# Performance work log

Measured on AMD Instinct MI355X. Metric: run time of the kernel, lower is better.

Reference implementation:

```python
import jax, jax.numpy as jnp
import numpy as np

MARGIN = 0.25
GAMMA = 256.0
NEG_INF = -1e30


def setup_inputs() -> dict:
    key = jax.random.key(0)
    k1, k2 = jax.random.split(key)
    B, D = 8192, 128
    return {
        "embeddings_a": jax.random.normal(k1, (B, D), dtype=jnp.float32),
        "embeddings_b": jax.random.normal(k2, (B, D), dtype=jnp.float32),
    }


def _l2_normalize(x, eps=1e-12):
    # matches F.normalize(p=2, dim=1): x / max(||x||, eps)
    n = jnp.sqrt(jnp.sum(x * x, axis=1, keepdims=True))
    return x / jnp.maximum(n, eps)


def reference(embeddings_a, embeddings_b):
    B = embeddings_a.shape[0]
    a = _l2_normalize(embeddings_a)
    b = _l2_normalize(embeddings_b)
    sim = a @ b.T  # [B, B]

    pos_mask = jnp.eye(B, dtype=bool)  # labels=None path

    # positive logits: -gamma * relu((1-m) - s) * (s - m)
    logit_pos = -GAMMA * jnp.maximum((1.0 - MARGIN) - sim, 0.0) * (sim - MARGIN)
    # negative logits:  gamma * relu(s - m) * (s + m)
    logit_neg = GAMMA * jnp.maximum(sim - MARGIN, 0.0) * (sim + MARGIN)

    # masked per-row logsumexp over positive / negative sets
    lse_pos = jax.nn.logsumexp(jnp.where(pos_mask, logit_pos, NEG_INF), axis=1)
    lse_neg = jax.nn.logsumexp(jnp.where(pos_mask, NEG_INF, logit_neg), axis=1)

    losses = jax.nn.softplus(lse_pos + lse_neg)  # [B]
    return jnp.mean(losses)  # reduction='mean'
```

## Files before the change

### kernel.cpp

```cpp
#include <hip/hip_runtime.h>


#define B_N 8192
#define D_K 128
#define MARGIN 0.25f
#define M2 (MARGIN * MARGIN)
#define GAMMA 256.0f

#define BM 256
#define BN 128
#define NCH 8
#define CPB (B_N / NCH)
#define NSUB (CPB / BN)
#define NROWBLK 32

typedef __attribute__((ext_vector_type(8))) short short8;
typedef __attribute__((ext_vector_type(4))) float f32x4;

__device__ __forceinline__ unsigned short f2bf(float x) {
  unsigned u = __float_as_uint(x);
  u += 0x7FFFu + ((u >> 16) & 1u);
  return (unsigned short)(u >> 16);
}

__device__ __forceinline__ void gload_lds16(const void* gsrc, void* ldst) {
  __builtin_amdgcn_global_load_lds(
      (const __attribute__((address_space(1))) void*)gsrc,
      (__attribute__((address_space(3))) void*)ldst, 16, 0, 0);
}

__global__ __launch_bounds__(256) void norm_diag_kernel(
    const float* __restrict__ a, const float* __restrict__ b,
    unsigned short* __restrict__ abf, unsigned short* __restrict__ bbf,
    float* __restrict__ diag) {
  int wave = threadIdx.x >> 6, lane = threadIdx.x & 63;
  int r = blockIdx.x * 4 + wave;
  int half = lane >> 5, l32 = lane & 31;
  const float* src = half ? b : a;
  unsigned short* dst = half ? bbf : abf;

  float4 v = ((const float4*)(src + (size_t)r * D_K))[l32];
  float ss = v.x * v.x + v.y * v.y + v.z * v.z + v.w * v.w;
  #pragma unroll
  for (int m = 16; m >= 1; m >>= 1) ss += __shfl_xor(ss, m);
  float inv = 1.0f / fmaxf(sqrtf(ss), 1e-12f);
  float n0 = v.x * inv, n1 = v.y * inv, n2 = v.z * inv, n3 = v.w * inv;

  ushort4 o = {f2bf(n0), f2bf(n1), f2bf(n2), f2bf(n3)};
  ((ushort4*)(dst + (size_t)r * D_K))[l32] = o;

  float d = n0 * __shfl_xor(n0, 32) + n1 * __shfl_xor(n1, 32) +
            n2 * __shfl_xor(n2, 32) + n3 * __shfl_xor(n3, 32);
  #pragma unroll
  for (int m = 16; m >= 1; m >>= 1) d += __shfl_xor(d, m);
  if (lane == 0) diag[r] = d;
}

__global__ __launch_bounds__(512, 2) void simlse_kernel(
    const unsigned short* __restrict__ abf, const unsigned short* __restrict__ bbf,
    float* __restrict__ partS) {
  __shared__ __align__(16) unsigned short BB[2][BN * D_K];
  __shared__ float sred[BM][2];

  const int tid = threadIdx.x;
  const int wave = tid >> 6, lane = tid & 63;
  const int r16 = lane & 15, kq = lane >> 4;
  const int wr = wave >> 1, wc = wave & 1;
  const int rowBase = blockIdx.y * BM;
  const int chunk = blockIdx.x;

  #pragma unroll
  for (int half = 0; half < 2; ++half) {
    const unsigned short* srcA = abf + (size_t)(rowBase + half * 128) * D_K;
    #pragma unroll
    for (int it = 0; it < 4; ++it) {
      int gb = it * 512 + wave * 64;
      int g = gb + lane;
      int row = g >> 4, sl = g & 15;
      int sls = sl ^ (row & 7);
      gload_lds16(srcA + (size_t)row * D_K + sls * 8, &BB[half][gb * 8]);
    }
  }
  __syncthreads();

  short8 af[4][4];
  {
    const unsigned short* Abuf = BB[wr >> 1];
    const int rbase = (wr & 1) * 64;
    #pragma unroll
    for (int mi = 0; mi < 4; ++mi) {
      int row = rbase + mi * 16 + r16;
      #pragma unroll
      for (int ks = 0; ks < 4; ++ks) {
        int slot = (ks * 4 + kq) ^ (row & 7);
        af[mi][ks] = *(const short8*)&Abuf[row * D_K + slot * 8];
      }
    }
  }
  __syncthreads();

  #pragma unroll
  for (int h = 0; h < 2; ++h) {
    const unsigned short* srcB = bbf + (size_t)(chunk * CPB + h * BN) * D_K;
    #pragma unroll
    for (int it = 0; it < 4; ++it) {
      int gb = it * 512 + wave * 64;
      int g = gb + lane;
      int row = g >> 4, sl = g & 15;
      int sls = sl ^ (row & 7);
      gload_lds16(srcB + (size_t)row * D_K + sls * 8, &BB[h][gb * 8]);
    }
  }
  __syncthreads();

  float Ssum[4][4];
  #pragma unroll
  for (int mi = 0; mi < 4; ++mi)
    #pragma unroll
    for (int r = 0; r < 4; ++r) Ssum[mi][r] = 0.0f;

  #pragma unroll 2
  for (int st = 0; st < NSUB; ++st) {
    const unsigned short* cb = BB[st & 1];

    f32x4 acc[4][4];
    const f32x4 z4 = {0.f, 0.f, 0.f, 0.f};
    #pragma unroll
    for (int mi = 0; mi < 4; ++mi)
      #pragma unroll
      for (int ni = 0; ni < 4; ++ni) acc[mi][ni] = z4;

    #pragma unroll
    for (int ks = 0; ks < 4; ++ks) {
      short8 bf[4];
      #pragma unroll
      for (int ni = 0; ni < 4; ++ni) {
        int row = wc * 64 + ni * 16 + r16;
        int slot = (ks * 4 + kq) ^ (row & 7);
        bf[ni] = *(const short8*)&cb[row * D_K + slot * 8];
      }
      #pragma unroll
      for (int mi = 0; mi < 4; ++mi)
        #pragma unroll
        for (int ni = 0; ni < 4; ++ni)
          acc[mi][ni] = __builtin_amdgcn_mfma_f32_16x16x32_bf16(
              af[mi][ks], bf[ni], acc[mi][ni], 0, 0, 0);
    }

    #pragma unroll
    for (int mi = 0; mi < 4; ++mi)
      #pragma unroll
      for (int ni = 0; ni < 4; ++ni) {
        f32x4 v = acc[mi][ni];
        float mx = fmaxf(fmaxf(v[0], v[1]), fmaxf(v[2], v[3]));
        if (__any(mx > MARGIN)) {
          #pragma unroll
          for (int r = 0; r < 4; ++r) {
            float s = v[r];
            float t = fmaf(s, s, -M2);
            float z = (s > MARGIN) ? GAMMA * t : 0.0f;
            Ssum[mi][r] += __expf(z) - 1.0f;
          }
        }
      }

    __syncthreads();

    if (st + 2 < NSUB) {
      const unsigned short* srcB =
          bbf + (size_t)(chunk * CPB + (st + 2) * BN) * D_K;
      unsigned short* dstB = (unsigned short*)BB[st & 1];
      #pragma unroll
      for (int it = 0; it < 4; ++it) {
        int gb = it * 512 + wave * 64;
        int g = gb + lane;
        int row = g >> 4, sl = g & 15;
        int sls = sl ^ (row & 7);
        gload_lds16(srcB + (size_t)row * D_K + sls * 8, &dstB[gb * 8]);
      }
    }
  }

  #pragma unroll
  for (int mi = 0; mi < 4; ++mi)
    #pragma unroll
    for (int r = 0; r < 4; ++r) {
      float v = Ssum[mi][r];
      v += __shfl_xor(v, 1);
      v += __shfl_xor(v, 2);
      v += __shfl_xor(v, 4);
      v += __shfl_xor(v, 8);
      if (r16 == 0) sred[wr * 64 + mi * 16 + kq * 4 + r][wc] = v;
    }
  __syncthreads();
  if (tid < BM)
    partS[(size_t)chunk * B_N + rowBase + tid] = sred[tid][0] + sred[tid][1];
}

__global__ __launch_bounds__(256) void rowfin_kernel(
    const float* __restrict__ partS, const float* __restrict__ diag,
    float* __restrict__ bpart) {
  __shared__ float red[4];
  int tid = threadIdx.x, lane = tid & 63, wid = tid >> 6;
  int i = blockIdx.x * 256 + tid;
  float S = 0.0f;
  #pragma unroll
  for (int c = 0; c < NCH; ++c) S += partS[(size_t)c * B_N + i];
  float sd = diag[i];
  float zd = (sd > MARGIN) ? GAMMA * fmaf(sd, sd, -M2) : 0.0f;
  float ed = __expf(zd);
  float lneg = __logf((float)B_N + S - ed);
  float lpos = -GAMMA * fmaxf((1.0f - MARGIN) - sd, 0.0f) * (sd - MARGIN);
  float x = lpos + lneg;
  float acc = fmaxf(x, 0.0f) + log1pf(__expf(-fabsf(x)));
  #pragma unroll
  for (int m = 32; m >= 1; m >>= 1) acc += __shfl_xor(acc, m);
  if (lane == 0) red[wid] = acc;
  __syncthreads();
  if (tid == 0) bpart[blockIdx.x] = red[0] + red[1] + red[2] + red[3];
}

__global__ __launch_bounds__(64) void mean_kernel(
    const float* __restrict__ bpart, float* __restrict__ out) {
  int lane = threadIdx.x;
  float v = (lane < 32) ? bpart[lane] : 0.0f;
  #pragma unroll
  for (int m = 32; m >= 1; m >>= 1) v += __shfl_xor(v, m);
  if (lane == 0) out[0] = v * (1.0f / B_N);
}

extern "C" void kernel_launch(void* const* d_in, const int* in_sizes, int n_in,
                              void* d_out, int out_size, void* d_ws, size_t ws_size,
                              hipStream_t stream) {
  const float* a = (const float*)d_in[0];
  const float* b = (const float*)d_in[1];
  float* out = (float*)d_out;

  char* w = (char*)d_ws;
  unsigned short* abf = (unsigned short*)w;
  unsigned short* bbf = (unsigned short*)(w + (size_t)B_N * D_K * 2);
  float* partS = (float*)(w + (size_t)B_N * D_K * 4);
  float* diag = partS + (size_t)NCH * B_N;
  float* bpart = diag + B_N;

  norm_diag_kernel<<<B_N / 4, 256, 0, stream>>>(a, b, abf, bbf, diag);
  simlse_kernel<<<dim3(NCH, B_N / BM), 512, 0, stream>>>(abf, bbf, partS);
  rowfin_kernel<<<NROWBLK, 256, 0, stream>>>(partS, diag, bpart);
  mean_kernel<<<1, 64, 0, stream>>>(bpart, out);
}
```

Measured before the change: 41.44 us.

## Fuse row finalize and mean into sim kernel via last-block atomic counters

Removes the separate rowfin and mean kernel launches. Each row-group keeps an atomic counter, and the last of its NCH chunk blocks computes the per-row losses and a block partial. A global counter then lets the last row-group block write the mean. Counters are zeroed in norm_diag_kernel. This cuts two launches and their gaps, at the cost of fences and atomics at the end of every sim block.

```diff
diff --git a/kernel.cpp b/kernel.cpp
--- a/kernel.cpp
+++ b/kernel.cpp
@@ -12,7 +12,7 @@
 #define NCH 8
 #define CPB (B_N / NCH)
 #define NSUB (CPB / BN)
-#define NROWBLK 32
+#define NYG (B_N / BM)
 
 typedef __attribute__((ext_vector_type(8))) short short8;
 typedef __attribute__((ext_vector_type(4))) float f32x4;
@@ -32,7 +32,8 @@
 __global__ __launch_bounds__(256) void norm_diag_kernel(
     const float* __restrict__ a, const float* __restrict__ b,
     unsigned short* __restrict__ abf, unsigned short* __restrict__ bbf,
-    float* __restrict__ diag) {
+    float* __restrict__ diag, int* __restrict__ cnt) {
+  if (blockIdx.x == 0 && threadIdx.x < NYG + 1) cnt[threadIdx.x] = 0;
   int wave = threadIdx.x >> 6, lane = threadIdx.x & 63;
   int r = blockIdx.x * 4 + wave;
   int half = lane >> 5, l32 = lane & 31;
@@ -56,11 +57,14 @@
   if (lane == 0) diag[r] = d;
 }
 
-__global__ __launch_bounds__(512, 2) void simlse_kernel(
+__global__ __launch_bounds__(512, 2) void simlse_fused_kernel(
     const unsigned short* __restrict__ abf, const unsigned short* __restrict__ bbf,
-    float* __restrict__ partS) {
+    const float* __restrict__ diag, float* __restrict__ partS,
+    float* __restrict__ bpart, int* __restrict__ cnt, float* __restrict__ out) {
   __shared__ __align__(16) unsigned short BB[2][BN * D_K];
   __shared__ float sred[BM][2];
+  __shared__ float redf[8];
+  __shared__ int amlast;
 
   const int tid = threadIdx.x;
   const int wave = tid >> 6, lane = tid & 63;
@@ -195,38 +199,51 @@
   __syncthreads();
   if (tid < BM)
     partS[(size_t)chunk * B_N + rowBase + tid] = sred[tid][0] + sred[tid][1];
-}
-
-__global__ __launch_bounds__(256) void rowfin_kernel(
-    const float* __restrict__ partS, const float* __restrict__ diag,
-    float* __restrict__ bpart) {
-  __shared__ float red[4];
-  int tid = threadIdx.x, lane = tid & 63, wid = tid >> 6;
-  int i = blockIdx.x * 256 + tid;
-  float S = 0.0f;
-  #pragma unroll
-  for (int c = 0; c < NCH; ++c) S += partS[(size_t)c * B_N + i];
-  float sd = diag[i];
-  float zd = (sd > MARGIN) ? GAMMA * fmaf(sd, sd, -M2) : 0.0f;
-  float ed = __expf(zd);
-  float lneg = __logf((float)B_N + S - ed);
-  float lpos = -GAMMA * fmaxf((1.0f - MARGIN) - sd, 0.0f) * (sd - MARGIN);
-  float x = lpos + lneg;
-  float acc = fmaxf(x, 0.0f) + log1pf(__expf(-fabsf(x)));
-  #pragma unroll
-  for (int m = 32; m >= 1; m >>= 1) acc += __shfl_xor(acc, m);
-  if (lane == 0) red[wid] = acc;
-  __syncthreads();
-  if (tid == 0) bpart[blockIdx.x] = red[0] + red[1] + red[2] + red[3];
-}
-
-__global__ __launch_bounds__(64) void mean_kernel(
-    const float* __restrict__ bpart, float* __restrict__ out) {
-  int lane = threadIdx.x;
-  float v = (lane < 32) ? bpart[lane] : 0.0f;
-  #pragma unroll
-  for (int m = 32; m >= 1; m >>= 1) v += __shfl_xor(v, m);
-  if (lane == 0) out[0] = v * (1.0f / B_N);
+
+  __threadfence();
+  if (tid == 0)
+    amlast = (__hip_atomic_fetch_add(&cnt[blockIdx.y], 1, __ATOMIC_ACQ_REL,
+                                     __HIP_MEMORY_SCOPE_AGENT) == NCH - 1);
+  __syncthreads();
+  if (!amlast) return;
+
+  float loss = 0.0f;
+  if (tid < BM) {
+    int row = rowBase + tid;
+    float S = 0.0f;
+    #pragma unroll
+    for (int c = 0; c < NCH; ++c)
+      S += __hip_atomic_load(&partS[(size_t)c * B_N + row], __ATOMIC_RELAXED,
+                             __HIP_MEMORY_SCOPE_AGENT);
+    float sd = diag[row];
+    float zd = (sd > MARGIN) ? GAMMA * fmaf(sd, sd, -M2) : 0.0f;
+    float ed = __expf(zd);
+    float lneg = __logf((float)B_N + S - ed);
+    float lpos = -GAMMA * fmaxf((1.0f - MARGIN) - sd, 0.0f) * (sd - MARGIN);
+    float x = lpos + lneg;
+    loss = fmaxf(x, 0.0f) + log1pf(__expf(-fabsf(x)));
+  }
+  #pragma unroll
+  for (int m = 32; m >= 1; m >>= 1) loss += __shfl_xor(loss, m);
+  if (lane == 0) redf[wave] = loss;
+  __syncthreads();
+  if (tid == 0) {
+    float t = 0.0f;
+    #pragma unroll
+    for (int i = 0; i < 8; ++i) t += redf[i];
+    bpart[blockIdx.y] = t;
+    __threadfence();
+    int old = __hip_atomic_fetch_add(&cnt[NYG], 1, __ATOMIC_ACQ_REL,
+                                     __HIP_MEMORY_SCOPE_AGENT);
+    if (old == NYG - 1) {
+      float tot = 0.0f;
+      #pragma unroll
+      for (int j = 0; j < NYG; ++j)
+        tot += __hip_atomic_load(&bpart[j], __ATOMIC_RELAXED,
+                                 __HIP_MEMORY_SCOPE_AGENT);
+      out[0] = tot * (1.0f / B_N);
+    }
+  }
 }
 
 extern "C" void kernel_launch(void* const* d_in, const int* in_sizes, int n_in,
@@ -242,9 +259,9 @@
   float* partS = (float*)(w + (size_t)B_N * D_K * 4);
   float* diag = partS + (size_t)NCH * B_N;
   float* bpart = diag + B_N;
-
-  norm_diag_kernel<<<B_N / 4, 256, 0, stream>>>(a, b, abf, bbf, diag);
-  simlse_kernel<<<dim3(NCH, B_N / BM), 512, 0, stream>>>(abf, bbf, partS);
-  rowfin_kernel<<<NROWBLK, 256, 0, stream>>>(partS, diag, bpart);
-  mean_kernel<<<1, 64, 0, stream>>>(bpart, out);
-}
+  int* cnt = (int*)(bpart + NYG);
+
+  norm_diag_kernel<<<B_N / 4, 256, 0, stream>>>(a, b, abf, bbf, diag, cnt);
+  simlse_fused_kernel<<<dim3(NCH, NYG), 512, 0, stream>>>(
+      abf, bbf, diag, partS, bpart, cnt, out);
+}
```

Measured after the change: 74.16 us. 79.0% more time.

## Shrink sim tile to 128 rows with single-buffered B and higher occupancy

Applied to the files above, without the earlier changes.

Halves the row tile to 128 and the workgroup to 256 threads. It replaces the double-buffered B tiles with one 32KB LDS buffer that is loaded synchronously at the top of each sub-tile iteration. Staging offsets are precomputed once, and launch bounds now target three blocks per CU. The aim is more resident blocks and more blocks in the grid (512 vs 256), so other blocks can hide load latency in place of in-block prefetch. The cost is losing the overlap between loading and compute inside a block, two barriers per iteration, and reading B from global memory twice as often.

```diff
diff --git a/kernel.cpp b/kernel.cpp
--- a/kernel.cpp
+++ b/kernel.cpp
@@ -7,7 +7,7 @@
 #define M2 (MARGIN * MARGIN)
 #define GAMMA 256.0f
 
-#define BM 256
+#define BM 128
 #define BN 128
 #define NCH 8
 #define CPB (B_N / NCH)
@@ -56,10 +56,10 @@
   if (lane == 0) diag[r] = d;
 }
 
-__global__ __launch_bounds__(512, 2) void simlse_kernel(
+__global__ __launch_bounds__(256, 3) void simlse_kernel(
     const unsigned short* __restrict__ abf, const unsigned short* __restrict__ bbf,
     float* __restrict__ partS) {
-  __shared__ __align__(16) unsigned short BB[2][BN * D_K];
+  __shared__ __align__(16) unsigned short Bs[BN * D_K];
   __shared__ float sred[BM][2];
 
   const int tid = threadIdx.x;
@@ -69,49 +69,32 @@
   const int rowBase = blockIdx.y * BM;
   const int chunk = blockIdx.x;
 
-  #pragma unroll
-  for (int half = 0; half < 2; ++half) {
-    const unsigned short* srcA = abf + (size_t)(rowBase + half * 128) * D_K;
-    #pragma unroll
-    for (int it = 0; it < 4; ++it) {
-      int gb = it * 512 + wave * 64;
-      int g = gb + lane;
-      int row = g >> 4, sl = g & 15;
-      int sls = sl ^ (row & 7);
-      gload_lds16(srcA + (size_t)row * D_K + sls * 8, &BB[half][gb * 8]);
-    }
+  int stageOff[8];
+  #pragma unroll
+  for (int it = 0; it < 8; ++it) {
+    int g = it * 256 + wave * 64 + lane;
+    int row = g >> 4, sl = g & 15;
+    stageOff[it] = row * D_K + (sl ^ (row & 7)) * 8;
+  }
+
+  {
+    const unsigned short* srcA = abf + (size_t)rowBase * D_K;
+    #pragma unroll
+    for (int it = 0; it < 8; ++it)
+      gload_lds16(srcA + stageOff[it], &Bs[(it * 256 + wave * 64) * 8]);
   }
   __syncthreads();
 
   short8 af[4][4];
-  {
-    const unsigned short* Abuf = BB[wr >> 1];
-    const int rbase = (wr & 1) * 64;
-    #pragma unroll
-    for (int mi = 0; mi < 4; ++mi) {
-      int row = rbase + mi * 16 + r16;
-      #pragma unroll
-      for (int ks = 0; ks < 4; ++ks) {
-        int slot = (ks * 4 + kq) ^ (row & 7);
-        af[mi][ks] = *(const short8*)&Abuf[row * D_K + slot * 8];
-      }
-    }
-  }
-  __syncthreads();
-
-  #pragma unroll
-  for (int h = 0; h < 2; ++h) {
-    const unsigned short* srcB = bbf + (size_t)(chunk * CPB + h * BN) * D_K;
-    #pragma unroll
-    for (int it = 0; it < 4; ++it) {
-      int gb = it * 512 + wave * 64;
-      int g = gb + lane;
-      int row = g >> 4, sl = g & 15;
-      int sls = sl ^ (row & 7);
-      gload_lds16(srcB + (size_t)row * D_K + sls * 8, &BB[h][gb * 8]);
-    }
-  }
-  __syncthreads();
+  #pragma unroll
+  for (int mi = 0; mi < 4; ++mi) {
+    int row = wr * 64 + mi * 16 + r16;
+    #pragma unroll
+    for (int ks = 0; ks < 4; ++ks) {
+      int slot = (ks * 4 + kq) ^ (row & 7);
+      af[mi][ks] = *(const short8*)&Bs[row * D_K + slot * 8];
+    }
+  }
 
   float Ssum[4][4];
   #pragma unroll
@@ -119,9 +102,15 @@
     #pragma unroll
     for (int r = 0; r < 4; ++r) Ssum[mi][r] = 0.0f;
 
-  #pragma unroll 2
   for (int st = 0; st < NSUB; ++st) {
-    const unsigned short* cb = BB[st & 1];
+    __syncthreads();
+    {
+      const unsigned short* srcB = bbf + (size_t)(chunk * CPB + st * BN) * D_K;
+      #pragma unroll
+      for (int it = 0; it < 8; ++it)
+        gload_lds16(srcB + stageOff[it], &Bs[(it * 256 + wave * 64) * 8]);
+    }
+    __syncthreads();
 
     f32x4 acc[4][4];
     const f32x4 z4 = {0.f, 0.f, 0.f, 0.f};
@@ -137,7 +126,7 @@
       for (int ni = 0; ni < 4; ++ni) {
         int row = wc * 64 + ni * 16 + r16;
         int slot = (ks * 4 + kq) ^ (row & 7);
-        bf[ni] = *(const short8*)&cb[row * D_K + slot * 8];
+        bf[ni] = *(const short8*)&Bs[row * D_K + slot * 8];
       }
       #pragma unroll
       for (int mi = 0; mi < 4; ++mi)
@@ -163,22 +152,6 @@
           }
         }
       }
-
-    __syncthreads();
-
-    if (st + 2 < NSUB) {
-      const unsigned short* srcB =
-          bbf + (size_t)(chunk * CPB + (st + 2) * BN) * D_K;
-      unsigned short* dstB = (unsigned short*)BB[st & 1];
-      #pragma unroll
-      for (int it = 0; it < 4; ++it) {
-        int gb = it * 512 + wave * 64;
-        int g = gb + lane;
-        int row = g >> 4, sl = g & 15;
-        int sls = sl ^ (row & 7);
-        gload_lds16(srcB + (size_t)row * D_K + sls * 8, &dstB[gb * 8]);
-      }
-    }
   }
 
   #pragma unroll
@@ -244,7 +217,7 @@
   float* bpart = diag + B_N;
 
   norm_diag_kernel<<<B_N / 4, 256, 0, stream>>>(a, b, abf, bbf, diag);
-  simlse_kernel<<<dim3(NCH, B_N / BM), 512, 0, stream>>>(abf, bbf, partS);
+  simlse_kernel<<<dim3(NCH, B_N / BM), 256, 0, stream>>>(abf, bbf, partS);
   rowfin_kernel<<<NROWBLK, 256, 0, stream>>>(partS, diag, bpart);
   mean_kernel<<<1, 64, 0, stream>>>(bpart, out);
 }
```

New measurement: 57.06 us. 37.7% more time.
